# Kernel optimization log

Measured on AMD Instinct MI355X. Metric: run time of the kernel, lower is better.

The kernel has to match this reference:

```python
import jax, jax.numpy as jnp
import numpy as np

B, BARS, BEATS, FRAC = 64, 16, 4, 8
IN_F = 10 * 47 * 2  # 940
LIN_OUT = 100
BEAT_H = 16
BAR_H = 32


def _p(key, shape, scale=0.05):
    return jax.random.normal(key, shape, dtype=jnp.float32) * scale


def setup_inputs() -> dict:
    key = jax.random.key(0)
    ks = jax.random.split(key, 16)
    return {
        "channels": jax.random.normal(ks[0], (B, BARS, BEATS, FRAC, 10, 2, 47), dtype=jnp.float32),
        "lin_w": _p(ks[1], (LIN_OUT, IN_F)),
        "lin_b": _p(ks[2], (LIN_OUT,)),
        # beats LSTM (unidirectional), PyTorch gate order i,f,g,o
        "b_wih": _p(ks[3], (4 * BEAT_H, LIN_OUT)),
        "b_whh": _p(ks[4], (4 * BEAT_H, BEAT_H)),
        "b_bih": _p(ks[5], (4 * BEAT_H,)),
        "b_bhh": _p(ks[6], (4 * BEAT_H,)),
        # bars LSTM, bidirectional: forward (f_) and reverse (r_) directions
        "f_wih": _p(ks[7], (4 * BAR_H, BEAT_H)),
        "f_whh": _p(ks[8], (4 * BAR_H, BAR_H)),
        "f_bih": _p(ks[9], (4 * BAR_H,)),
        "f_bhh": _p(ks[10], (4 * BAR_H,)),
        "r_wih": _p(ks[11], (4 * BAR_H, BEAT_H)),
        "r_whh": _p(ks[12], (4 * BAR_H, BAR_H)),
        "r_bih": _p(ks[13], (4 * BAR_H,)),
        "r_bhh": _p(ks[14], (4 * BAR_H,)),
    }


def lstm(x, wih, whh, bih, bhh):
    """PyTorch-semantics LSTM, batch_first. x: [N, T, F] -> h_seq [N, T, H]."""
    N = x.shape[0]
    H = whh.shape[1]
    # precompute input contribution for all timesteps
    xg = jnp.einsum('ntf,gf->ntg', x, wih) + (bih + bhh)  # [N, T, 4H]

    def step(carry, xt):
        h, c = carry
        gates = xt + h @ whh.T  # [N, 4H]
        i, f, g, o = jnp.split(gates, 4, axis=-1)
        c = jax.nn.sigmoid(f) * c + jax.nn.sigmoid(i) * jnp.tanh(g)
        h = jax.nn.sigmoid(o) * jnp.tanh(c)
        return (h, c), h

    h0 = jnp.zeros((N, H), x.dtype)
    _, hs = jax.lax.scan(step, (h0, h0), jnp.swapaxes(xg, 0, 1))  # [T, N, H]
    return jnp.swapaxes(hs, 0, 1)


def bilstm(x, f_wih, f_whh, f_bih, f_bhh, r_wih, r_whh, r_bih, r_bhh):
    fwd = lstm(x, f_wih, f_whh, f_bih, f_bhh)
    bwd = jnp.flip(lstm(jnp.flip(x, axis=1), r_wih, r_whh, r_bih, r_bhh), axis=1)
    return jnp.concatenate([fwd, bwd], axis=-1)


def reference(channels, lin_w, lin_b,
              b_wih, b_whh, b_bih, b_bhh,
              f_wih, f_whh, f_bih, f_bhh,
              r_wih, r_whh, r_bih, r_bhh):
    # channels: [B, bars, beats, frac, 10, 2, 47]
    x = jnp.swapaxes(channels, -1, -2)  # [..., 10, 47, 2]
    x = x.reshape(*x.shape[:4], IN_F)   # squash dims 4..6 -> 940
    x = jax.nn.relu(x @ lin_w.T + lin_b)  # [B, bars, beats, frac, 100]

    # Distributed depth=2: fold (B, bars, beats) into batch, seq over frac
    xb = x.reshape(B * BARS * BEATS, FRAC, LIN_OUT)
    beats = lstm(xb, b_wih, b_whh, b_bih, b_bhh)
    beats = beats.reshape(B, BARS, BEATS, FRAC, BEAT_H)

    # last fraction hidden state, then Distributed depth=1 over beats axis
    xl = beats[:, :, :, -1].reshape(B * BARS, BEATS, BEAT_H)
    bars = bilstm(xl, f_wih, f_whh, f_bih, f_bhh, r_wih, r_whh, r_bih, r_bhh)
    bars = bars.reshape(B, BARS, BEATS, 2 * BAR_H)
    return beats, bars
```

## Files before the change

kernel.cpp:

```cpp
#include <hip/hip_runtime.h>
#include <hip/hip_bf16.h>

typedef float f32x4 __attribute__((ext_vector_type(4)));
typedef short bf16x8 __attribute__((ext_vector_type(8)));

#define MFMA16(a, b, c) __builtin_amdgcn_mfma_f32_16x16x32_bf16(a, b, c, 0, 0, 0)

constexpr int K1      = 940;
constexpr int KP2     = 1024;
constexpr int NP      = 112;
constexpr int OUT1_LD = 128;

__device__ __forceinline__ float sigf(float x) { return 1.f / (1.f + __expf(-x)); }
__device__ __forceinline__ float tanhfast(float x) { return 2.f / (1.f + __expf(-2.f * x)) - 1.f; }

__device__ __forceinline__ short f2b(float x) {
  __hip_bfloat16 b = __float2bfloat16(x);
  return *reinterpret_cast<short*>(&b);
}

__global__ void prep_kernel(const float* __restrict__ lin_w,
                            const float* __restrict__ b_wih,
                            __hip_bfloat16* __restrict__ w2,
                            __hip_bfloat16* __restrict__ bw2) {
  int idx = blockIdx.x * 256 + threadIdx.x;
  if (idx < NP * KP2) {
    int n = idx >> 10, k = idx & 1023;
    float v = 0.f;
    if (n < 100 && k < K1) {
      int c10 = k / 94, rem = k - c10 * 94;
      int c2 = rem / 47, c47 = rem - c2 * 47;
      int f = c10 * 94 + c47 * 2 + c2;
      v = lin_w[n * K1 + f];
    }
    w2[idx] = __float2bfloat16(v);
  } else {
    int i2 = idx - NP * KP2;
    if (i2 < 64 * 128) {
      int g = i2 >> 7, k = i2 & 127;
      bw2[i2] = __float2bfloat16((k < 100) ? b_wih[g * 100 + k] : 0.f);
    }
  }
}

__global__ __launch_bounds__(512, 2)
void linear_relu_splitk(const float* __restrict__ ch,
                        const __hip_bfloat16* __restrict__ w2,
                        const float* __restrict__ lin_b,
                        __hip_bfloat16* __restrict__ out1) {
  __shared__ float red[8 * 16 * NP];
  const int tid = threadIdx.x;
  const int w = tid >> 6, lane = tid & 63;
  const int l16 = lane & 15, bq = lane >> 4;
  const int kbase = w * 128;

  bf16x8 breg[4][7];
#pragma unroll
  for (int s = 0; s < 4; ++s)
#pragma unroll
    for (int nt = 0; nt < 7; ++nt)
      breg[s][nt] = *reinterpret_cast<const bf16x8*>(
          &w2[(nt * 16 + l16) * KP2 + kbase + s * 32 + bq * 8]);

  const int mbase = blockIdx.x * 64;

  auto issueA = [&](int m0, float4* buf) {
    const float* ar = ch + (long)(m0 + l16) * K1 + kbase + bq * 8;
    if (w < 7) {
#pragma unroll
      for (int s = 0; s < 4; ++s) {
        buf[2 * s]     = *reinterpret_cast<const float4*>(ar + s * 32);
        buf[2 * s + 1] = *reinterpret_cast<const float4*>(ar + s * 32 + 4);
      }
    } else {
      buf[0] = *reinterpret_cast<const float4*>(ar);
      buf[1] = *reinterpret_cast<const float4*>(ar + 4);
      float t[8];
#pragma unroll
      for (int j = 0; j < 8; ++j) {
        int k = 928 + bq * 8 + j;
        t[j] = (k < K1) ? ar[32 + j] : 0.f;
      }
      buf[2] = float4{t[0], t[1], t[2], t[3]};
      buf[3] = float4{t[4], t[5], t[6], t[7]};
      buf[4] = buf[5] = buf[6] = buf[7] = float4{0.f, 0.f, 0.f, 0.f};
    }
  };

  float4 a0[8], a1[8];
  issueA(mbase, a0);

#pragma unroll
  for (int i = 0; i < 4; ++i) {
    float4* cur = (i & 1) ? a1 : a0;
    float4* nxt = (i & 1) ? a0 : a1;
    if (i < 3) issueA(mbase + (i + 1) * 16, nxt);

    f32x4 acc[7] = {};
#pragma unroll
    for (int s = 0; s < 4; ++s) {
      float4 lo = cur[2 * s], hi = cur[2 * s + 1];
      bf16x8 a = bf16x8{f2b(lo.x), f2b(lo.y), f2b(lo.z), f2b(lo.w),
                        f2b(hi.x), f2b(hi.y), f2b(hi.z), f2b(hi.w)};
#pragma unroll
      for (int nt = 0; nt < 7; ++nt) acc[nt] = MFMA16(a, breg[s][nt], acc[nt]);
    }

#pragma unroll
    for (int nt = 0; nt < 7; ++nt)
#pragma unroll
      for (int r = 0; r < 4; ++r)
        red[(w * 16 + bq * 4 + r) * NP + nt * 16 + l16] = acc[nt][r];
    __syncthreads();

    const int m0 = mbase + i * 16;
    if (tid < 448) {
      const int col = tid % NP;
      const int rb = (tid / NP) * 4;
      const float bias = (col < 100) ? lin_b[col] : 0.f;
#pragma unroll
      for (int r = 0; r < 4; ++r) {
        float s = 0.f;
#pragma unroll
        for (int ww = 0; ww < 8; ++ww) s += red[(ww * 16 + rb + r) * NP + col];
        float v = fmaxf(s + bias, 0.f);
        out1[(m0 + rb + r) * OUT1_LD + col] = __float2bfloat16((col < 100) ? v : 0.f);
      }
    } else {
      const int t2 = tid - 448;
      const int row = t2 >> 2, c0 = 112 + (t2 & 3) * 4;
#pragma unroll
      for (int q = 0; q < 4; ++q)
        out1[(m0 + row) * OUT1_LD + c0 + q] = __float2bfloat16(0.f);
    }
    __syncthreads();
  }
}

__global__ __launch_bounds__(256)
void xg_mfma(const __hip_bfloat16* __restrict__ out1,
             const __hip_bfloat16* __restrict__ bw2,
             const float* __restrict__ bih,
             const float* __restrict__ bhh,
             float* __restrict__ xg) {
  const int tid = threadIdx.x;
  const int wave = tid >> 6, lane = tid & 63;
  const int l16 = lane & 15, bq = lane >> 4;
  const int m0 = blockIdx.x * 64 + wave * 16;
  const int arow = (m0 + l16) * OUT1_LD;
  f32x4 acc[4] = {};
#pragma unroll
  for (int s = 0; s < 4; ++s) {
    const int k0 = s * 32;
    bf16x8 a = *reinterpret_cast<const bf16x8*>(&out1[arow + k0 + bq * 8]);
#pragma unroll
    for (int nt = 0; nt < 4; ++nt) {
      bf16x8 b = *reinterpret_cast<const bf16x8*>(&bw2[(nt * 16 + l16) * 128 + k0 + bq * 8]);
      acc[nt] = MFMA16(a, b, acc[nt]);
    }
  }
  const int mb = m0 + bq * 4;
#pragma unroll
  for (int nt = 0; nt < 4; ++nt) {
    const int g = nt * 16 + l16;
    const float bias = bih[g] + bhh[g];
#pragma unroll
    for (int r = 0; r < 4; ++r) xg[(mb + r) * 64 + g] = acc[nt][r] + bias;
  }
}

__global__ __launch_bounds__(256)
void beats_lstm(const float* __restrict__ xg,
                const float* __restrict__ whh,
                float* __restrict__ beats) {
  const int lane = threadIdx.x & 63;
  const int seq = blockIdx.x * 4 + (threadIdx.x >> 6);
  const int cell = lane & 15;
  float wr[16];
#pragma unroll
  for (int u = 0; u < 16; ++u) wr[u] = whh[lane * 16 + u];
  const float* xs = xg + seq * 512;
  float xv[8];
#pragma unroll
  for (int t = 0; t < 8; ++t) xv[t] = xs[t * 64 + lane];
  float h[16];
#pragma unroll
  for (int u = 0; u < 16; ++u) h[u] = 0.f;
  float c = 0.f;
#pragma unroll
  for (int t = 0; t < 8; ++t) {
    float pre = xv[t];
#pragma unroll
    for (int u = 0; u < 16; ++u) pre += wr[u] * h[u];
    float act = (lane >= 32 && lane < 48) ? tanhfast(pre) : sigf(pre);
    float gi = __shfl(act, cell);
    float gf = __shfl(act, cell + 16);
    float gg = __shfl(act, cell + 32);
    float go = __shfl(act, cell + 48);
    c = gf * c + gi * gg;
    float hn = go * tanhfast(c);
#pragma unroll
    for (int u = 0; u < 16; ++u) h[u] = __shfl(hn, u);
    if (lane < 16) beats[seq * 128 + t * 16 + lane] = hn;
  }
}

__global__ __launch_bounds__(256)
void bars_bilstm(const float* __restrict__ fwih, const float* __restrict__ fwhh,
                 const float* __restrict__ fbih, const float* __restrict__ fbhh,
                 const float* __restrict__ rwih, const float* __restrict__ rwhh,
                 const float* __restrict__ rbih, const float* __restrict__ rbhh,
                 const float* __restrict__ beats,
                 float* __restrict__ bars) {
  const int tid = threadIdx.x;
  const int dir = tid >> 7, g = tid & 127;
  const int n = blockIdx.x;
  const float* wih = dir ? rwih : fwih;
  const float* whh = dir ? rwhh : fwhh;
  const float bias = dir ? (rbih[g] + rbhh[g]) : (fbih[g] + fbhh[g]);
  float wi[16], wh[32];
#pragma unroll
  for (int u = 0; u < 16; ++u) wi[u] = wih[g * 16 + u];
#pragma unroll
  for (int u = 0; u < 32; ++u) wh[u] = whh[g * 32 + u];
  __shared__ float xbuf[2][16];
  __shared__ float hbuf[2][32];
  __shared__ float gact[2][128];
  float c = 0.f;
  if (g < 32) hbuf[dir][g] = 0.f;
  __syncthreads();
  for (int t = 0; t < 4; ++t) {
    const int tt = dir ? (3 - t) : t;
    if (g < 16) xbuf[dir][g] = beats[((n * 4 + tt) * 8 + 7) * 16 + g];
    __syncthreads();
    float pre = bias;
#pragma unroll
    for (int u = 0; u < 16; ++u) pre += wi[u] * xbuf[dir][u];
#pragma unroll
    for (int u = 0; u < 32; ++u) pre += wh[u] * hbuf[dir][u];
    gact[dir][g] = (g >= 64 && g < 96) ? tanhfast(pre) : sigf(pre);
    __syncthreads();
    if (g < 32) {
      c = gact[dir][32 + g] * c + gact[dir][g] * gact[dir][64 + g];
      float hn = gact[dir][96 + g] * tanhfast(c);
      hbuf[dir][g] = hn;
      bars[(n * 4 + tt) * 64 + dir * 32 + g] = hn;
    }
    __syncthreads();
  }
}

extern "C" void kernel_launch(void* const* d_in, const int* in_sizes, int n_in,
                              void* d_out, int out_size, void* d_ws, size_t ws_size,
                              hipStream_t stream) {
  const float* ch    = (const float*)d_in[0];
  const float* lin_w = (const float*)d_in[1];
  const float* lin_b = (const float*)d_in[2];
  const float* b_wih = (const float*)d_in[3];
  const float* b_whh = (const float*)d_in[4];
  const float* b_bih = (const float*)d_in[5];
  const float* b_bhh = (const float*)d_in[6];
  const float* f_wih = (const float*)d_in[7];
  const float* f_whh = (const float*)d_in[8];
  const float* f_bih = (const float*)d_in[9];
  const float* f_bhh = (const float*)d_in[10];
  const float* r_wih = (const float*)d_in[11];
  const float* r_whh = (const float*)d_in[12];
  const float* r_bih = (const float*)d_in[13];
  const float* r_bhh = (const float*)d_in[14];

  char* ws = (char*)d_ws;
  __hip_bfloat16* w2   = (__hip_bfloat16*)ws;
  __hip_bfloat16* bw2  = (__hip_bfloat16*)(ws + 229376);
  __hip_bfloat16* out1 = (__hip_bfloat16*)(ws + 245760);
  float*          xg   = (float*)(ws + 8634368);
  float*          out  = (float*)d_out;

  prep_kernel<<<480, 256, 0, stream>>>(lin_w, b_wih, w2, bw2);
  linear_relu_splitk<<<512, 512, 0, stream>>>(ch, w2, lin_b, out1);
  xg_mfma<<<512, 256, 0, stream>>>(out1, bw2, b_bih, b_bhh, xg);
  beats_lstm<<<1024, 256, 0, stream>>>(xg, b_whh, out);
  bars_bilstm<<<1024, 256, 0, stream>>>(f_wih, f_whh, f_bih, f_bhh,
                                        r_wih, r_whh, r_bih, r_bhh,
                                        out, out + 524288);
}
```

Before: 244.3 us.

## Fuse linear, input-gate GEMM and beats LSTM into one kernel via LDS

Merges the linear+ReLU split-K kernel, the xg MFMA projection and the beats LSTM into a single kernel. Each block keeps its 64 rows of linear output in shared memory, computes the gate preactivations into shared memory, then runs 8 LSTM sequences (one per wave). This removes the global round trips for out1 and xg and two kernel launches. In exchange it uses more LDS per block, which may reduce occupancy of the memory-bound linear stage.

Result: no change. 240.3 us (-1.6%).

```diff
diff --git a/kernel.cpp b/kernel.cpp
--- a/kernel.cpp
+++ b/kernel.cpp
@@ -6,10 +6,10 @@
 
 #define MFMA16(a, b, c) __builtin_amdgcn_mfma_f32_16x16x32_bf16(a, b, c, 0, 0, 0)
 
-constexpr int K1      = 940;
-constexpr int KP2     = 1024;
-constexpr int NP      = 112;
-constexpr int OUT1_LD = 128;
+constexpr int K1  = 940;
+constexpr int KP2 = 1024;
+constexpr int NP  = 112;
+constexpr int OSL = 136;
 
 __device__ __forceinline__ float sigf(float x) { return 1.f / (1.f + __expf(-x)); }
 __device__ __forceinline__ float tanhfast(float x) { return 2.f / (1.f + __expf(-2.f * x)) - 1.f; }
@@ -44,11 +44,17 @@
 }
 
 __global__ __launch_bounds__(512, 2)
-void linear_relu_splitk(const float* __restrict__ ch,
-                        const __hip_bfloat16* __restrict__ w2,
-                        const float* __restrict__ lin_b,
-                        __hip_bfloat16* __restrict__ out1) {
+void fused_encoder(const float* __restrict__ ch,
+                   const __hip_bfloat16* __restrict__ w2,
+                   const float* __restrict__ lin_b,
+                   const __hip_bfloat16* __restrict__ bw2,
+                   const float* __restrict__ bih,
+                   const float* __restrict__ bhh,
+                   const float* __restrict__ whh,
+                   float* __restrict__ beats) {
   __shared__ float red[8 * 16 * NP];
+  __shared__ __align__(16) __hip_bfloat16 out_s[64 * OSL];
+  __shared__ float xg_s[64 * 65];
   const int tid = threadIdx.x;
   const int w = tid >> 6, lane = tid & 63;
   const int l16 = lane & 15, bq = lane >> 4;
@@ -113,7 +119,6 @@
         red[(w * 16 + bq * 4 + r) * NP + nt * 16 + l16] = acc[nt][r];
     __syncthreads();
 
-    const int m0 = mbase + i * 16;
     if (tid < 448) {
       const int col = tid % NP;
       const int rb = (tid / NP) * 4;
@@ -124,84 +129,74 @@
 #pragma unroll
         for (int ww = 0; ww < 8; ++ww) s += red[(ww * 16 + rb + r) * NP + col];
         float v = fmaxf(s + bias, 0.f);
-        out1[(m0 + rb + r) * OUT1_LD + col] = __float2bfloat16((col < 100) ? v : 0.f);
+        out_s[(i * 16 + rb + r) * OSL + col] = __float2bfloat16((col < 100) ? v : 0.f);
       }
     } else {
       const int t2 = tid - 448;
       const int row = t2 >> 2, c0 = 112 + (t2 & 3) * 4;
 #pragma unroll
       for (int q = 0; q < 4; ++q)
-        out1[(m0 + row) * OUT1_LD + c0 + q] = __float2bfloat16(0.f);
-    }
-    __syncthreads();
-  }
-}
-
-__global__ __launch_bounds__(256)
-void xg_mfma(const __hip_bfloat16* __restrict__ out1,
-             const __hip_bfloat16* __restrict__ bw2,
-             const float* __restrict__ bih,
-             const float* __restrict__ bhh,
-             float* __restrict__ xg) {
-  const int tid = threadIdx.x;
-  const int wave = tid >> 6, lane = tid & 63;
-  const int l16 = lane & 15, bq = lane >> 4;
-  const int m0 = blockIdx.x * 64 + wave * 16;
-  const int arow = (m0 + l16) * OUT1_LD;
-  f32x4 acc[4] = {};
-#pragma unroll
-  for (int s = 0; s < 4; ++s) {
-    const int k0 = s * 32;
-    bf16x8 a = *reinterpret_cast<const bf16x8*>(&out1[arow + k0 + bq * 8]);
-#pragma unroll
-    for (int nt = 0; nt < 4; ++nt) {
-      bf16x8 b = *reinterpret_cast<const bf16x8*>(&bw2[(nt * 16 + l16) * 128 + k0 + bq * 8]);
-      acc[nt] = MFMA16(a, b, acc[nt]);
-    }
-  }
-  const int mb = m0 + bq * 4;
-#pragma unroll
-  for (int nt = 0; nt < 4; ++nt) {
-    const int g = nt * 16 + l16;
-    const float bias = bih[g] + bhh[g];
-#pragma unroll
-    for (int r = 0; r < 4; ++r) xg[(mb + r) * 64 + g] = acc[nt][r] + bias;
-  }
-}
-
-__global__ __launch_bounds__(256)
-void beats_lstm(const float* __restrict__ xg,
-                const float* __restrict__ whh,
-                float* __restrict__ beats) {
-  const int lane = threadIdx.x & 63;
-  const int seq = blockIdx.x * 4 + (threadIdx.x >> 6);
-  const int cell = lane & 15;
-  float wr[16];
-#pragma unroll
-  for (int u = 0; u < 16; ++u) wr[u] = whh[lane * 16 + u];
-  const float* xs = xg + seq * 512;
-  float xv[8];
-#pragma unroll
-  for (int t = 0; t < 8; ++t) xv[t] = xs[t * 64 + lane];
-  float h[16];
-#pragma unroll
-  for (int u = 0; u < 16; ++u) h[u] = 0.f;
-  float c = 0.f;
-#pragma unroll
-  for (int t = 0; t < 8; ++t) {
-    float pre = xv[t];
-#pragma unroll
-    for (int u = 0; u < 16; ++u) pre += wr[u] * h[u];
-    float act = (lane >= 32 && lane < 48) ? tanhfast(pre) : sigf(pre);
-    float gi = __shfl(act, cell);
-    float gf = __shfl(act, cell + 16);
-    float gg = __shfl(act, cell + 32);
-    float go = __shfl(act, cell + 48);
-    c = gf * c + gi * gg;
-    float hn = go * tanhfast(c);
-#pragma unroll
-    for (int u = 0; u < 16; ++u) h[u] = __shfl(hn, u);
-    if (lane < 16) beats[seq * 128 + t * 16 + lane] = hn;
+        out_s[(i * 16 + row) * OSL + c0 + q] = __float2bfloat16(0.f);
+    }
+    __syncthreads();
+  }
+
+  {
+    const int rt = w >> 1, gt0 = (w & 1) * 2;
+    bf16x8 av[4];
+#pragma unroll
+    for (int s = 0; s < 4; ++s)
+      av[s] = *reinterpret_cast<const bf16x8*>(&out_s[(rt * 16 + l16) * OSL + s * 32 + bq * 8]);
+    f32x4 xacc[2] = {{0.f, 0.f, 0.f, 0.f}, {0.f, 0.f, 0.f, 0.f}};
+#pragma unroll
+    for (int g2 = 0; g2 < 2; ++g2) {
+      const int gt = gt0 + g2;
+#pragma unroll
+      for (int s = 0; s < 4; ++s) {
+        bf16x8 b = *reinterpret_cast<const bf16x8*>(&bw2[(gt * 16 + l16) * 128 + s * 32 + bq * 8]);
+        xacc[g2] = MFMA16(av[s], b, xacc[g2]);
+      }
+    }
+#pragma unroll
+    for (int g2 = 0; g2 < 2; ++g2) {
+      const int gate = (gt0 + g2) * 16 + l16;
+      const float bias = bih[gate] + bhh[gate];
+#pragma unroll
+      for (int r = 0; r < 4; ++r)
+        xg_s[(rt * 16 + bq * 4 + r) * 65 + gate] = xacc[g2][r] + bias;
+    }
+  }
+  __syncthreads();
+
+  {
+    const int cell = lane & 15;
+    float wr[16];
+#pragma unroll
+    for (int u = 0; u < 16; ++u) wr[u] = whh[lane * 16 + u];
+    float xv[8];
+#pragma unroll
+    for (int t = 0; t < 8; ++t) xv[t] = xg_s[(w * 8 + t) * 65 + lane];
+    float h[16];
+#pragma unroll
+    for (int u = 0; u < 16; ++u) h[u] = 0.f;
+    float c = 0.f;
+    const int seq = blockIdx.x * 8 + w;
+#pragma unroll
+    for (int t = 0; t < 8; ++t) {
+      float pre = xv[t];
+#pragma unroll
+      for (int u = 0; u < 16; ++u) pre += wr[u] * h[u];
+      float act = (lane >= 32 && lane < 48) ? tanhfast(pre) : sigf(pre);
+      float gi = __shfl(act, cell);
+      float gf = __shfl(act, cell + 16);
+      float gg = __shfl(act, cell + 32);
+      float go = __shfl(act, cell + 48);
+      c = gf * c + gi * gg;
+      float hn = go * tanhfast(c);
+#pragma unroll
+      for (int u = 0; u < 16; ++u) h[u] = __shfl(hn, u);
+      if (lane < 16) beats[seq * 128 + t * 16 + lane] = hn;
+    }
   }
 }
 
@@ -270,16 +265,13 @@
   const float* r_bhh = (const float*)d_in[14];
 
   char* ws = (char*)d_ws;
-  __hip_bfloat16* w2   = (__hip_bfloat16*)ws;
-  __hip_bfloat16* bw2  = (__hip_bfloat16*)(ws + 229376);
-  __hip_bfloat16* out1 = (__hip_bfloat16*)(ws + 245760);
-  float*          xg   = (float*)(ws + 8634368);
-  float*          out  = (float*)d_out;
+  __hip_bfloat16* w2  = (__hip_bfloat16*)ws;
+  __hip_bfloat16* bw2 = (__hip_bfloat16*)(ws + 229376);
+  float*          out = (float*)d_out;
 
   prep_kernel<<<480, 256, 0, stream>>>(lin_w, b_wih, w2, bw2);
-  linear_relu_splitk<<<512, 512, 0, stream>>>(ch, w2, lin_b, out1);
-  xg_mfma<<<512, 256, 0, stream>>>(out1, bw2, b_bih, b_bhh, xg);
-  beats_lstm<<<1024, 256, 0, stream>>>(xg, b_whh, out);
+  fused_encoder<<<512, 512, 0, stream>>>(ch, w2, lin_b, bw2, b_bih, b_bhh,
+                                         b_whh, out);
   bars_bilstm<<<1024, 256, 0, stream>>>(f_wih, f_whh, f_bih, f_bhh,
                                         r_wih, r_whh, r_bih, r_bhh,
                                         out, out + 524288);
```
